# Kernel tuning notes

Hardware: AMD Instinct MI355X
Metric: run time of the kernel (lower is better)

## Reference

```python
import jax, jax.numpy as jnp
import numpy as np

TEMPERATURE = 12.5      # EMDLayer temperature
SINKHORN_EPS = 0.05     # entropic regularization for the batched EMD solve
SINKHORN_ITERS = 50     # fixed iteration count (jit-friendly)
WEIGHT_EPS = 1e-05      # OpenCVSolver adds 1e-5 after relu


def setup_inputs() -> dict:
    key = jax.random.key(0)
    k1, k2, k3 = jax.random.split(key, 3)
    E, Q, W, N = 4, 75, 5, 64
    similarity_map = jax.random.uniform(k1, (E, Q, W, N, N), dtype=jnp.float32)
    weight_1 = jax.random.uniform(k2, (E, Q, W, N), dtype=jnp.float32)
    weight_2 = jax.random.uniform(k3, (E, W, Q, N), dtype=jnp.float32)
    return {"similarity_map": similarity_map, "weight_1": weight_1, "weight_2": weight_2}


def _emd_flow(cost, a, b):
    """Batched entropic-regularized EMD (log-domain Sinkhorn).
    cost: [B, N, N]; a, b: [B, N] positive marginals (each sums to N).
    Returns flow: [B, N, N] with row sums ~a and col sums ~b."""
    logK = -cost / SINKHORN_EPS            # [B, N, N]
    log_a = jnp.log(a)
    log_b = jnp.log(b)

    def step(carry, _):
        log_u, log_v = carry
        log_u = log_a - jax.scipy.special.logsumexp(logK + log_v[:, None, :], axis=2)
        log_v = log_b - jax.scipy.special.logsumexp(logK + log_u[:, :, None], axis=1)
        return (log_u, log_v), None

    init = (jnp.zeros_like(log_a), jnp.zeros_like(log_b))
    (log_u, log_v), _ = jax.lax.scan(step, init, None, length=SINKHORN_ITERS)
    return jnp.exp(logK + log_u[:, :, None] + log_v[:, None, :])


def reference(similarity_map, weight_1, weight_2):
    E, Q, W, N, _ = similarity_map.shape
    sim = similarity_map.reshape(-1, N, N)                       # [B, N, N]
    w1 = weight_1.reshape(-1, N)                                  # [B, N]
    w2 = jnp.transpose(weight_2, (0, 2, 1, 3)).reshape(-1, N)     # transpose(1,2) then flatten

    # OpenCVSolver weight preprocessing: relu + eps, renormalize to sum N
    w1 = jax.nn.relu(w1) + WEIGHT_EPS
    w1 = w1 * (N / jnp.sum(w1, axis=1, keepdims=True))
    w2 = jax.nn.relu(w2) + WEIGHT_EPS
    w2 = w2 * (N / jnp.sum(w2, axis=1, keepdims=True))

    cost = 1.0 - sim
    flow = _emd_flow(cost, w1, w2)                                # [B, N, N]
    scores = jnp.sum(flow * sim, axis=(-1, -2)).reshape(E, Q, W)
    return scores * (TEMPERATURE / N)
```

## Files before the change

kernel.cpp:

```cpp
#include <hip/hip_runtime.h>

#define N 64
#define ITERS 50
#define TEMP 12.5f
#define WEPS 1e-5f
#define QDIM 75
#define WDIM 5

typedef float v2f __attribute__((ext_vector_type(2)));

static __device__ __forceinline__ v2f pkfma(v2f a, v2f b, v2f c) {
    v2f d;
    asm("v_pk_fma_f32 %0, %1, %2, %3" : "=v"(d) : "v"(a), "v"(b), "v"(c));
    return d;
}

#define DPP_XOR1(x) __int_as_float(__builtin_amdgcn_update_dpp(0, __float_as_int(x), 0xB1, 0xF, 0xF, true))
#define DPP_XOR2(x) __int_as_float(__builtin_amdgcn_update_dpp(0, __float_as_int(x), 0x4E, 0xF, 0xF, true))

__device__ __forceinline__ float waveReduceSum(float x) {
#pragma unroll
    for (int off = 32; off; off >>= 1) x += __shfl_xor(x, off, 64);
    return x;
}

__global__ __launch_bounds__(64, 1) void emd_pk(
    const float* __restrict__ sim,
    const float* __restrict__ w1,
    const float* __restrict__ w2,
    float* __restrict__ out,
    int B)
{
    __shared__ __align__(16) float S[128];

    const int lane = threadIdx.x;
    const int b    = blockIdx.x;
    const int g    = lane >> 2;
    const int s    = lane & 3;
    const float* gm = sim + (size_t)b * N * N;

    v2f Kr2[4][8], Kc2[4][8];
#pragma unroll
    for (int k = 0; k < 4; ++k)
#pragma unroll
        for (int m = 0; m < 4; ++m) {
            float4 x = *(const float4*)(gm + (4 * g + k) * N + 16 * s + 4 * m);
            Kr2[k][2 * m + 0][0] = __expf((x.x - 1.0f) * 20.0f);
            Kr2[k][2 * m + 0][1] = __expf((x.y - 1.0f) * 20.0f);
            Kr2[k][2 * m + 1][0] = __expf((x.z - 1.0f) * 20.0f);
            Kr2[k][2 * m + 1][1] = __expf((x.w - 1.0f) * 20.0f);
        }
#pragma unroll
    for (int j = 0; j < 16; ++j) {
        float4 x = *(const float4*)(gm + (16 * s + j) * N + 4 * g);
        Kc2[0][j >> 1][j & 1] = __expf((x.x - 1.0f) * 20.0f);
        Kc2[1][j >> 1][j & 1] = __expf((x.y - 1.0f) * 20.0f);
        Kc2[2][j >> 1][j & 1] = __expf((x.z - 1.0f) * 20.0f);
        Kc2[3][j >> 1][j & 1] = __expf((x.w - 1.0f) * 20.0f);
    }
#pragma unroll
    for (int k = 0; k < 4; ++k)
#pragma unroll
        for (int m = 0; m < 8; ++m) {
            asm volatile("" : "+v"(Kr2[k][m]));
            asm volatile("" : "+v"(Kc2[k][m]));
        }

    float a_own = w1[(size_t)b * N + lane];
    a_own = fmaxf(a_own, 0.0f) + WEPS;
    a_own *= (float)N / waveReduceSum(a_own);

    const int e  = b / (QDIM * WDIM);
    const int rm = b % (QDIM * WDIM);
    const int q  = rm / WDIM, w = rm % WDIM;
    float b_own = w2[((((size_t)e * WDIM + w) * QDIM) + q) * N + lane];
    b_own = fmaxf(b_own, 0.0f) + WEPS;
    b_own *= (float)N / waveReduceSum(b_own);

    S[64 + lane] = 1.0f;
    __syncthreads();

    float u = 0.0f;
#pragma unroll 1
    for (int it = 0; it < ITERS; ++it) {
        {
            const float4* V4 = (const float4*)&S[64 + 16 * s];
            float4 x0 = V4[0], x1 = V4[1], x2 = V4[2], x3 = V4[3];
            v2f vv[8] = {{x0.x, x0.y}, {x0.z, x0.w}, {x1.x, x1.y}, {x1.z, x1.w},
                         {x2.x, x2.y}, {x2.z, x2.w}, {x3.x, x3.y}, {x3.z, x3.w}};
            v2f acc0 = {0, 0}, acc1 = {0, 0}, acc2 = {0, 0}, acc3 = {0, 0};
#pragma unroll
            for (int m = 0; m < 8; ++m) {
                acc0 = pkfma(Kr2[0][m], vv[m], acc0);
                acc1 = pkfma(Kr2[1][m], vv[m], acc1);
                acc2 = pkfma(Kr2[2][m], vv[m], acc2);
                acc3 = pkfma(Kr2[3][m], vv[m], acc3);
            }
            float s0 = acc0[0] + acc0[1], s1 = acc1[0] + acc1[1];
            float s2 = acc2[0] + acc2[1], s3 = acc3[0] + acc3[1];
            s0 += DPP_XOR1(s0); s1 += DPP_XOR1(s1); s2 += DPP_XOR1(s2); s3 += DPP_XOR1(s3);
            s0 += DPP_XOR2(s0); s1 += DPP_XOR2(s1); s2 += DPP_XOR2(s2); s3 += DPP_XOR2(s3);
            float ab = (s & 1) ? s1 : s0;
            float cd = (s & 1) ? s3 : s2;
            float se = (s & 2) ? cd : ab;
            u = a_own * __builtin_amdgcn_rcpf(se);
            S[lane] = u;
        }
        __syncthreads();

        {
            const float4* U4 = (const float4*)&S[16 * s];
            float4 x0 = U4[0], x1 = U4[1], x2 = U4[2], x3 = U4[3];
            v2f uu[8] = {{x0.x, x0.y}, {x0.z, x0.w}, {x1.x, x1.y}, {x1.z, x1.w},
                         {x2.x, x2.y}, {x2.z, x2.w}, {x3.x, x3.y}, {x3.z, x3.w}};
            v2f acc0 = {0, 0}, acc1 = {0, 0}, acc2 = {0, 0}, acc3 = {0, 0};
#pragma unroll
            for (int m = 0; m < 8; ++m) {
                acc0 = pkfma(Kc2[0][m], uu[m], acc0);
                acc1 = pkfma(Kc2[1][m], uu[m], acc1);
                acc2 = pkfma(Kc2[2][m], uu[m], acc2);
                acc3 = pkfma(Kc2[3][m], uu[m], acc3);
            }
            float s0 = acc0[0] + acc0[1], s1 = acc1[0] + acc1[1];
            float s2 = acc2[0] + acc2[1], s3 = acc3[0] + acc3[1];
            s0 += DPP_XOR1(s0); s1 += DPP_XOR1(s1); s2 += DPP_XOR1(s2); s3 += DPP_XOR1(s3);
            s0 += DPP_XOR2(s0); s1 += DPP_XOR2(s1); s2 += DPP_XOR2(s2); s3 += DPP_XOR2(s3);
            float ab = (s & 1) ? s1 : s0;
            float cd = (s & 1) ? s3 : s2;
            float se = (s & 2) ? cd : ab;
            S[64 + lane] = b_own * __builtin_amdgcn_rcpf(se);
        }
        __syncthreads();
    }

    {
        float4 u4 = *(const float4*)&S[4 * g];
        const float4* V4 = (const float4*)&S[64 + 16 * s];
        float4 x0 = V4[0], x1 = V4[1], x2 = V4[2], x3 = V4[3];
        float vj[16] = {x0.x, x0.y, x0.z, x0.w, x1.x, x1.y, x1.z, x1.w,
                        x2.x, x2.y, x2.z, x2.w, x3.x, x3.y, x3.z, x3.w};
        float uk[4] = {u4.x, u4.y, u4.z, u4.w};
        const float c = 0.69314718056f / 20.0f;
        float p = 0.0f;
#pragma unroll
        for (int k = 0; k < 4; ++k) {
            float rs = 0.0f;
#pragma unroll
            for (int j = 0; j < 16; ++j) {
                float kk = Kr2[k][j >> 1][j & 1];
                float sv = fmaf(__log2f(kk), c, 1.0f);
                rs = fmaf(kk * sv, vj[j], rs);
            }
            p = fmaf(uk[k], rs, p);
        }
        float tot = waveReduceSum(p);
        if (lane == 0) out[b] = tot * (TEMP / (float)N);
    }
}

extern "C" void kernel_launch(void* const* d_in, const int* in_sizes, int n_in,
                              void* d_out, int out_size, void* d_ws, size_t ws_size,
                              hipStream_t stream) {
    const float* sim = (const float*)d_in[0];
    const float* w1  = (const float*)d_in[1];
    const float* w2  = (const float*)d_in[2];
    float* out       = (float*)d_out;
    const int B = in_sizes[0] / (N * N);
    emd_pk<<<B, 64, 0, stream>>>(sim, w1, w2, out, B);
}
```

Measured before the change: 99.98 us.

## Split each Sinkhorn problem across two waves with half the kernel rows each

Each block now uses 128 threads (two waves), and each thread holds 2 rows/columns of the exponentiated kernel instead of 4, halving per-thread FMA work and register use per iteration. The marginal preprocessing is split across the two waves and staged through shared memory. The final score is reduced across both waves via shared memory. This shortens the serial per-iteration dependency chain in exchange for cross-wave barriers and doubling the thread count, and the barriers may cost more than the work they remove.

Measured after the change: 105.5 us. +5.6%, slower.

```diff
diff --git a/kernel.cpp b/kernel.cpp
--- a/kernel.cpp
+++ b/kernel.cpp
@@ -24,27 +24,46 @@
     return x;
 }
 
-__global__ __launch_bounds__(64, 1) void emd_pk(
+__global__ __launch_bounds__(128, 1) void emd_pk2(
     const float* __restrict__ sim,
     const float* __restrict__ w1,
     const float* __restrict__ w2,
     float* __restrict__ out,
     int B)
 {
-    __shared__ __align__(16) float S[128];
+    __shared__ __align__(16) float U[N], V[N], A[N], Bm[N];
+    __shared__ float Wred[2];
 
-    const int lane = threadIdx.x;
+    const int t    = threadIdx.x;
+    const int lane = t & 63;
+    const int wv   = t >> 6;
+    const int g    = t >> 2;
+    const int s    = t & 3;
     const int b    = blockIdx.x;
-    const int g    = lane >> 2;
-    const int s    = lane & 3;
     const float* gm = sim + (size_t)b * N * N;
 
-    v2f Kr2[4][8], Kc2[4][8];
+    if (wv == 0) {
+        float a = w1[(size_t)b * N + lane];
+        a = fmaxf(a, 0.0f) + WEPS;
+        a *= (float)N / waveReduceSum(a);
+        A[lane] = a;
+        V[lane] = 1.0f;
+    } else {
+        const int e  = b / (QDIM * WDIM);
+        const int rm = b % (QDIM * WDIM);
+        const int q  = rm / WDIM, w = rm % WDIM;
+        float gg = w2[((((size_t)e * WDIM + w) * QDIM) + q) * N + lane];
+        gg = fmaxf(gg, 0.0f) + WEPS;
+        gg *= (float)N / waveReduceSum(gg);
+        Bm[lane] = gg;
+    }
+
+    v2f Kr2[2][8], Kc2[2][8];
 #pragma unroll
-    for (int k = 0; k < 4; ++k)
+    for (int k = 0; k < 2; ++k)
 #pragma unroll
         for (int m = 0; m < 4; ++m) {
-            float4 x = *(const float4*)(gm + (4 * g + k) * N + 16 * s + 4 * m);
+            float4 x = *(const float4*)(gm + (2 * g + k) * N + 16 * s + 4 * m);
             Kr2[k][2 * m + 0][0] = __expf((x.x - 1.0f) * 20.0f);
             Kr2[k][2 * m + 0][1] = __expf((x.y - 1.0f) * 20.0f);
             Kr2[k][2 * m + 1][0] = __expf((x.z - 1.0f) * 20.0f);
@@ -52,98 +71,87 @@
         }
 #pragma unroll
     for (int j = 0; j < 16; ++j) {
-        float4 x = *(const float4*)(gm + (16 * s + j) * N + 4 * g);
+        float2 x = *(const float2*)(gm + (16 * s + j) * N + 2 * g);
         Kc2[0][j >> 1][j & 1] = __expf((x.x - 1.0f) * 20.0f);
         Kc2[1][j >> 1][j & 1] = __expf((x.y - 1.0f) * 20.0f);
-        Kc2[2][j >> 1][j & 1] = __expf((x.z - 1.0f) * 20.0f);
-        Kc2[3][j >> 1][j & 1] = __expf((x.w - 1.0f) * 20.0f);
     }
 #pragma unroll
-    for (int k = 0; k < 4; ++k)
+    for (int k = 0; k < 2; ++k)
 #pragma unroll
         for (int m = 0; m < 8; ++m) {
             asm volatile("" : "+v"(Kr2[k][m]));
             asm volatile("" : "+v"(Kc2[k][m]));
         }
 
-    float a_own = w1[(size_t)b * N + lane];
-    a_own = fmaxf(a_own, 0.0f) + WEPS;
-    a_own *= (float)N / waveReduceSum(a_own);
+    __syncthreads();
+    const float2 a2 = *(const float2*)&A[2 * g];
+    const float2 b2 = *(const float2*)&Bm[2 * g];
 
-    const int e  = b / (QDIM * WDIM);
-    const int rm = b % (QDIM * WDIM);
-    const int q  = rm / WDIM, w = rm % WDIM;
-    float b_own = w2[((((size_t)e * WDIM + w) * QDIM) + q) * N + lane];
-    b_own = fmaxf(b_own, 0.0f) + WEPS;
-    b_own *= (float)N / waveReduceSum(b_own);
-
-    S[64 + lane] = 1.0f;
-    __syncthreads();
-
-    float u = 0.0f;
 #pragma unroll 1
     for (int it = 0; it < ITERS; ++it) {
         {
-            const float4* V4 = (const float4*)&S[64 + 16 * s];
+            const float4* V4 = (const float4*)&V[16 * s];
             float4 x0 = V4[0], x1 = V4[1], x2 = V4[2], x3 = V4[3];
             v2f vv[8] = {{x0.x, x0.y}, {x0.z, x0.w}, {x1.x, x1.y}, {x1.z, x1.w},
                          {x2.x, x2.y}, {x2.z, x2.w}, {x3.x, x3.y}, {x3.z, x3.w}};
-            v2f acc0 = {0, 0}, acc1 = {0, 0}, acc2 = {0, 0}, acc3 = {0, 0};
+            v2f a00 = {0, 0}, a01 = {0, 0}, a10 = {0, 0}, a11 = {0, 0};
 #pragma unroll
-            for (int m = 0; m < 8; ++m) {
-                acc0 = pkfma(Kr2[0][m], vv[m], acc0);
-                acc1 = pkfma(Kr2[1][m], vv[m], acc1);
-                acc2 = pkfma(Kr2[2][m], vv[m], acc2);
-                acc3 = pkfma(Kr2[3][m], vv[m], acc3);
+            for (int m = 0; m < 4; ++m) {
+                a00 = pkfma(Kr2[0][2 * m + 0], vv[2 * m + 0], a00);
+                a01 = pkfma(Kr2[0][2 * m + 1], vv[2 * m + 1], a01);
+                a10 = pkfma(Kr2[1][2 * m + 0], vv[2 * m + 0], a10);
+                a11 = pkfma(Kr2[1][2 * m + 1], vv[2 * m + 1], a11);
             }
-            float s0 = acc0[0] + acc0[1], s1 = acc1[0] + acc1[1];
-            float s2 = acc2[0] + acc2[1], s3 = acc3[0] + acc3[1];
-            s0 += DPP_XOR1(s0); s1 += DPP_XOR1(s1); s2 += DPP_XOR1(s2); s3 += DPP_XOR1(s3);
-            s0 += DPP_XOR2(s0); s1 += DPP_XOR2(s1); s2 += DPP_XOR2(s2); s3 += DPP_XOR2(s3);
-            float ab = (s & 1) ? s1 : s0;
-            float cd = (s & 1) ? s3 : s2;
-            float se = (s & 2) ? cd : ab;
-            u = a_own * __builtin_amdgcn_rcpf(se);
-            S[lane] = u;
+            float r0 = (a00[0] + a00[1]) + (a01[0] + a01[1]);
+            float r1 = (a10[0] + a10[1]) + (a11[0] + a11[1]);
+            r0 += DPP_XOR1(r0);  r1 += DPP_XOR1(r1);
+            r0 += DPP_XOR2(r0);  r1 += DPP_XOR2(r1);
+            if (s == 0) {
+                float2 uo;
+                uo.x = a2.x * __builtin_amdgcn_rcpf(r0);
+                uo.y = a2.y * __builtin_amdgcn_rcpf(r1);
+                *(float2*)&U[2 * g] = uo;
+            }
         }
         __syncthreads();
 
         {
-            const float4* U4 = (const float4*)&S[16 * s];
+            const float4* U4 = (const float4*)&U[16 * s];
             float4 x0 = U4[0], x1 = U4[1], x2 = U4[2], x3 = U4[3];
             v2f uu[8] = {{x0.x, x0.y}, {x0.z, x0.w}, {x1.x, x1.y}, {x1.z, x1.w},
                          {x2.x, x2.y}, {x2.z, x2.w}, {x3.x, x3.y}, {x3.z, x3.w}};
-            v2f acc0 = {0, 0}, acc1 = {0, 0}, acc2 = {0, 0}, acc3 = {0, 0};
+            v2f a00 = {0, 0}, a01 = {0, 0}, a10 = {0, 0}, a11 = {0, 0};
 #pragma unroll
-            for (int m = 0; m < 8; ++m) {
-                acc0 = pkfma(Kc2[0][m], uu[m], acc0);
-                acc1 = pkfma(Kc2[1][m], uu[m], acc1);
-                acc2 = pkfma(Kc2[2][m], uu[m], acc2);
-                acc3 = pkfma(Kc2[3][m], uu[m], acc3);
+            for (int m = 0; m < 4; ++m) {
+                a00 = pkfma(Kc2[0][2 * m + 0], uu[2 * m + 0], a00);
+                a01 = pkfma(Kc2[0][2 * m + 1], uu[2 * m + 1], a01);
+                a10 = pkfma(Kc2[1][2 * m + 0], uu[2 * m + 0], a10);
+                a11 = pkfma(Kc2[1][2 * m + 1], uu[2 * m + 1], a11);
             }
-            float s0 = acc0[0] + acc0[1], s1 = acc1[0] + acc1[1];
-            float s2 = acc2[0] + acc2[1], s3 = acc3[0] + acc3[1];
-            s0 += DPP_XOR1(s0); s1 += DPP_XOR1(s1); s2 += DPP_XOR1(s2); s3 += DPP_XOR1(s3);
-            s0 += DPP_XOR2(s0); s1 += DPP_XOR2(s1); s2 += DPP_XOR2(s2); s3 += DPP_XOR2(s3);
-            float ab = (s & 1) ? s1 : s0;
-            float cd = (s & 1) ? s3 : s2;
-            float se = (s & 2) ? cd : ab;
-            S[64 + lane] = b_own * __builtin_amdgcn_rcpf(se);
+            float r0 = (a00[0] + a00[1]) + (a01[0] + a01[1]);
+            float r1 = (a10[0] + a10[1]) + (a11[0] + a11[1]);
+            r0 += DPP_XOR1(r0);  r1 += DPP_XOR1(r1);
+            r0 += DPP_XOR2(r0);  r1 += DPP_XOR2(r1);
+            if (s == 0) {
+                float2 vo;
+                vo.x = b2.x * __builtin_amdgcn_rcpf(r0);
+                vo.y = b2.y * __builtin_amdgcn_rcpf(r1);
+                *(float2*)&V[2 * g] = vo;
+            }
         }
         __syncthreads();
     }
 
     {
-        float4 u4 = *(const float4*)&S[4 * g];
-        const float4* V4 = (const float4*)&S[64 + 16 * s];
+        const float2 u2 = *(const float2*)&U[2 * g];
+        const float4* V4 = (const float4*)&V[16 * s];
         float4 x0 = V4[0], x1 = V4[1], x2 = V4[2], x3 = V4[3];
         float vj[16] = {x0.x, x0.y, x0.z, x0.w, x1.x, x1.y, x1.z, x1.w,
                         x2.x, x2.y, x2.z, x2.w, x3.x, x3.y, x3.z, x3.w};
-        float uk[4] = {u4.x, u4.y, u4.z, u4.w};
         const float c = 0.69314718056f / 20.0f;
         float p = 0.0f;
 #pragma unroll
-        for (int k = 0; k < 4; ++k) {
+        for (int k = 0; k < 2; ++k) {
             float rs = 0.0f;
 #pragma unroll
             for (int j = 0; j < 16; ++j) {
@@ -151,11 +159,13 @@
                 float sv = fmaf(__log2f(kk), c, 1.0f);
                 rs = fmaf(kk * sv, vj[j], rs);
             }
-            p = fmaf(uk[k], rs, p);
+            p = fmaf(k ? u2.y : u2.x, rs, p);
         }
-        float tot = waveReduceSum(p);
-        if (lane == 0) out[b] = tot * (TEMP / (float)N);
+        float ws = waveReduceSum(p);
+        if (lane == 0) Wred[wv] = ws;
     }
+    __syncthreads();
+    if (t == 0) out[b] = (Wred[0] + Wred[1]) * (TEMP / (float)N);
 }
 
 extern "C" void kernel_launch(void* const* d_in, const int* in_sizes, int n_in,
@@ -166,5 +176,5 @@
     const float* w2  = (const float*)d_in[2];
     float* out       = (float*)d_out;
     const int B = in_sizes[0] / (N * N);
-    emd_pk<<<B, 64, 0, stream>>>(sim, w1, w2, out, B);
+    emd_pk2<<<B, 128, 0, stream>>>(sim, w1, w2, out, B);
 }
```
